# Performance work log

Hardware: AMD Instinct MI355X
Metric: run time of the kernel (lower is better)

## Reference

```python
import jax, jax.numpy as jnp
import numpy as np

B, S, D, N, NC = 2, 1024, 1024, 8192, 8


def _srw_chunked(x, h, emb_norm, tau_offset, w_read, w_write, n_chunks):
    Bd, Sd, Dd = x.shape
    Nd = emb_norm.shape[0]
    cs = Nd // n_chunks
    h_bf = h.astype(jnp.bfloat16)
    x_bf = x.astype(jnp.bfloat16)
    emb_bf = emb_norm.astype(jnp.bfloat16)
    read_bf = w_read.astype(jnp.bfloat16)
    write_bf = w_write.astype(jnp.bfloat16)
    z1 = jnp.zeros((Bd, Sd, 1))

    @jax.checkpoint
    def estimate_stats(h, emb, nc_val):
        ec0 = jax.lax.dynamic_slice_in_dim(emb, 0, cs, axis=0)
        sc0 = h @ ec0.T
        s_sum = sc0.sum(axis=-1, keepdims=True).astype(jnp.float32) * nc_val
        sq_sum = (sc0 ** 2).sum(axis=-1, keepdims=True).astype(jnp.float32) * nc_val
        return (s_sum, sq_sum)

    s_sum, sq_sum = estimate_stats(h_bf, emb_bf, n_chunks)
    s_mean = s_sum / Nd
    s_std = jnp.sqrt(sq_sum / Nd - s_mean ** 2) + 1e-08
    tau = s_mean + tau_offset * s_std
    tau_bf = tau.astype(jnp.bfloat16)

    @jax.checkpoint
    def gsrw_step(carry, i):
        out, es, em, ac, lbs, lbq = carry
        s = i * cs
        ec = jax.lax.dynamic_slice_in_dim(emb_bf, s, cs, axis=0)
        rc = jax.lax.dynamic_slice_in_dim(read_bf, s, cs, axis=0)
        wc = jax.lax.dynamic_slice_in_dim(write_bf, s, cs, axis=0)
        sc = h_bf @ ec.T  # [B,S,cs]
        raw = sc - tau_bf
        gc = jnp.where(raw > 0, raw, (1e-06 * jnp.exp(jnp.clip(raw.astype(jnp.float32), -10.0, 0.0))).astype(jnp.bfloat16))
        gc = jnp.clip(gc, 0.0, 10.0)
        eg = (jnp.exp(gc.astype(jnp.float32)) - 1.0).astype(jnp.bfloat16)
        ef = eg.astype(jnp.float32)
        xr = x_bf @ rc.T  # [B,S,cs]
        co = ((eg * xr) @ wc).astype(jnp.float32)  # [B,S,D]
        gn = ef.mean(axis=(0, 1))
        lbs = lbs + gn.sum()
        lbq = lbq + (gn ** 2).sum()
        return ((out + co,
                 es + ef.sum(axis=-1, keepdims=True),
                 jnp.maximum(em, ef.max(axis=-1, keepdims=True)),
                 ac + (raw > 0).sum(axis=-1, keepdims=True).astype(jnp.float32),
                 lbs, lbq), None)

    z_scalar = jnp.float32(0.0)
    init = (jnp.zeros((Bd, Sd, Dd), dtype=jnp.float32), z1,
            jnp.full((Bd, Sd, 1), -1000000000.0), z1, z_scalar, z_scalar)
    (raw_out, tes, tem, tac, lb_sum, lb_sq), _ = jax.lax.scan(gsrw_step, init, jnp.arange(n_chunks))
    inv_es = (1.0 / (tes + 1e-08)).astype(jnp.bfloat16)
    gs = jnp.tanh(tem).astype(jnp.bfloat16)
    out = raw_out * inv_es * gs
    exp_sum_scalar = tes.mean() + 1e-08
    norm_lb_sum = lb_sum / exp_sum_scalar
    norm_lb_sq = lb_sq / exp_sum_scalar ** 2
    lb_loss = norm_lb_sq * Nd - 2.0 * norm_lb_sum + 1.0
    gs_mean = jnp.tanh(tem).mean()
    es_mean = tes.mean()
    return (out.astype(jnp.float32), tac / Nd, tem, lb_loss, gs_mean, es_mean)


def setup_inputs() -> dict:
    key = jax.random.key(0)
    k = jax.random.split(key, 6)
    x = jax.random.normal(k[0], (B, S, D), jnp.float32)
    h = jax.random.normal(k[1], (B, S, D), jnp.float32)
    emb = jax.random.normal(k[2], (N, D), jnp.float32) * 0.02
    w_read = jax.random.normal(k[3], (N, D), jnp.float32) * 0.02
    w_write = jax.random.normal(k[4], (N, D), jnp.float32) * 0.02
    tau_offset = jax.random.normal(k[5], (B, S, 1), jnp.float32) * 0.1
    return {"x": x, "h": h, "emb": emb, "tau_offset": tau_offset,
            "w_read": w_read, "w_write": w_write, "n_chunks": NC}


def reference(x, h, emb, tau_offset, w_read, w_write, n_chunks):
    # caller (_know_forward) unit-normalizes the embedding pool first
    emb_norm = emb / (jnp.linalg.norm(emb, axis=-1, keepdims=True) + 1e-08)
    out, active_frac, gate_max, lb_loss, gs_mean, es_mean = _srw_chunked(
        x, h, emb_norm, tau_offset, w_read, w_write, n_chunks)
    return out
```

## Files before the change

kernel.cpp:

```cpp
#include <hip/hip_runtime.h>


#define MDIM 2048
#define DDIM 1024
#define NDIM 8192

typedef __attribute__((ext_vector_type(8))) __bf16 bf16x8;
typedef __attribute__((ext_vector_type(4))) float f32x4;

static __device__ __forceinline__ unsigned short f2b(float f) {
  unsigned u = __float_as_uint(f);
  u = (u + 0x7FFFu + ((u >> 16) & 1u)) >> 16;
  return (unsigned short)u;
}
static __device__ __forceinline__ float b2f(unsigned short s) {
  return __uint_as_float(((unsigned)s) << 16);
}


static __device__ __forceinline__ void stage_half(const unsigned short* __restrict__ src,
                                                  int ld, int row0, int k0,
                                                  char* lds, int lds_off, int w, int l) {
  const int rsub = l >> 3;
  const int col = k0 + 8 * ((l & 7) ^ rsub);
#pragma unroll
  for (int j = 0; j < 2; ++j) {
    const unsigned short* g =
        src + (size_t)(row0 + w * 8 + j * 64 + rsub) * (size_t)ld + col;
    __builtin_amdgcn_global_load_lds(
        (const __attribute__((address_space(1))) unsigned int*)(const void*)g,
        (__attribute__((address_space(3))) unsigned int*)(void*)(lds + lds_off + j * 8192 + w * 1024),
        16, 0, 0);
  }
}

#define LDSF(off) (*(const bf16x8*)(lds + (off)))
#define MFMA_BF16 __builtin_amdgcn_mfma_f32_16x16x32_bf16

static __device__ __forceinline__ void gemm256(const unsigned short* __restrict__ asrc,
                                               const unsigned short* __restrict__ bsrc,
                                               int ld, int m0, int n0, int kbase,
                                               char* lds, f32x4 (&acc)[8][4],
                                               int w, int l, int wr, int wc) {
  const int lrow = l & 15, lk = l >> 4;
  const int axor = (l & 7) << 4;
  const int kx0 = (lk << 4) ^ axor;
  const int kx1 = (64 | (lk << 4)) ^ axor;
  const int arow_off = lrow * 128;
  const int brow_off = ((wc & 1) * 64 + lrow) * 128;

  stage_half(asrc, ld, m0,       kbase,      lds, 0,             w, l);
  stage_half(asrc, ld, m0 + 128, kbase,      lds, 16384,         w, l);
  stage_half(bsrc, ld, n0,       kbase,      lds, 32768,         w, l);
  stage_half(bsrc, ld, n0 + 128, kbase,      lds, 49152,         w, l);
  stage_half(bsrc, ld, n0,       kbase + 64, lds, 65536 + 32768, w, l);
  stage_half(bsrc, ld, n0 + 128, kbase + 64, lds, 65536 + 49152, w, l);
  asm volatile("s_waitcnt vmcnt(4)" ::: "memory");
  __builtin_amdgcn_s_barrier();

  bf16x8 a[4][2], blo[2][2], bhi[2][2];
#pragma unroll 2
  for (int s = 0; s < 16; ++s) {
    const int ab = (s & 1) * 65536 + wr * 16384;
    const int bb = (s & 1) * 65536 + 32768 + (wc >> 1) * 16384;
#pragma unroll
    for (int m = 0; m < 4; ++m) {
      a[m][0] = LDSF(ab + arow_off + m * 2048 + kx0);
      a[m][1] = LDSF(ab + arow_off + m * 2048 + kx1);
    }
#pragma unroll
    for (int n = 0; n < 2; ++n) {
      blo[n][0] = LDSF(bb + brow_off + n * 2048 + kx0);
      blo[n][1] = LDSF(bb + brow_off + n * 2048 + kx1);
    }
    if (s + 1 < 16)
      stage_half(asrc, ld, m0, kbase + (s + 1) * 64, lds, ((s + 1) & 1) * 65536, w, l);
    asm volatile("s_waitcnt lgkmcnt(8)" ::: "memory");
    __builtin_amdgcn_s_barrier();
    asm volatile("s_waitcnt lgkmcnt(0)" ::: "memory");
    __builtin_amdgcn_s_setprio(1);
#pragma unroll
    for (int ks = 0; ks < 2; ++ks)
#pragma unroll
      for (int n = 0; n < 2; ++n)
#pragma unroll
        for (int m = 0; m < 4; ++m)
          acc[m][n] = MFMA_BF16(a[m][ks], blo[n][ks], acc[m][n], 0, 0, 0);
    __builtin_amdgcn_s_setprio(0);
    __builtin_amdgcn_s_barrier();
#pragma unroll
    for (int n = 0; n < 2; ++n) {
      bhi[n][0] = LDSF(bb + brow_off + (n + 2) * 2048 + kx0);
      bhi[n][1] = LDSF(bb + brow_off + (n + 2) * 2048 + kx1);
    }
    if (s + 1 < 16)
      stage_half(asrc, ld, m0 + 128, kbase + (s + 1) * 64, lds,
                 ((s + 1) & 1) * 65536 + 16384, w, l);
    __builtin_amdgcn_s_barrier();
    asm volatile("s_waitcnt lgkmcnt(0)" ::: "memory");
    __builtin_amdgcn_s_setprio(1);
#pragma unroll
    for (int ks = 0; ks < 2; ++ks)
#pragma unroll
      for (int n = 0; n < 2; ++n)
#pragma unroll
        for (int m = 0; m < 4; ++m)
          acc[m][n + 2] = MFMA_BF16(a[m][ks], bhi[n][ks], acc[m][n + 2], 0, 0, 0);
    __builtin_amdgcn_s_setprio(0);
    __builtin_amdgcn_s_barrier();
#pragma unroll
    for (int m = 0; m < 4; ++m) {
      a[m][0] = LDSF(ab + arow_off + (m + 4) * 2048 + kx0);
      a[m][1] = LDSF(ab + arow_off + (m + 4) * 2048 + kx1);
    }
    if (s + 2 < 16)
      stage_half(bsrc, ld, n0, kbase + (s + 2) * 64, lds, (s & 1) * 65536 + 32768, w, l);
    __builtin_amdgcn_s_barrier();
    asm volatile("s_waitcnt lgkmcnt(0)" ::: "memory");
    __builtin_amdgcn_s_setprio(1);
#pragma unroll
    for (int ks = 0; ks < 2; ++ks)
#pragma unroll
      for (int n = 0; n < 2; ++n)
#pragma unroll
        for (int m = 0; m < 4; ++m)
          acc[m + 4][n + 2] = MFMA_BF16(a[m][ks], bhi[n][ks], acc[m + 4][n + 2], 0, 0, 0);
    __builtin_amdgcn_s_setprio(0);
    __builtin_amdgcn_s_barrier();
    if (s + 2 < 16)
      stage_half(bsrc, ld, n0 + 128, kbase + (s + 2) * 64, lds, (s & 1) * 65536 + 49152, w, l);
    __builtin_amdgcn_s_barrier();
    asm volatile("s_waitcnt lgkmcnt(0)" ::: "memory");
    __builtin_amdgcn_s_setprio(1);
#pragma unroll
    for (int ks = 0; ks < 2; ++ks)
#pragma unroll
      for (int n = 0; n < 2; ++n)
#pragma unroll
        for (int m = 0; m < 4; ++m)
          acc[m + 4][n] = MFMA_BF16(a[m][ks], blo[n][ks], acc[m + 4][n], 0, 0, 0);
    __builtin_amdgcn_s_setprio(0);
    if (s <= 13) {
      asm volatile("s_waitcnt vmcnt(4)" ::: "memory");
    } else if (s == 14) {
      asm volatile("s_waitcnt vmcnt(0)" ::: "memory");
    }
    __builtin_amdgcn_s_barrier();
  }
}


__global__ __launch_bounds__(256) void k_norm(const float* __restrict__ emb,
                                              unsigned short* __restrict__ eb) {
  const int n = blockIdx.x, t = threadIdx.x;
  const float4 v = ((const float4*)(emb + (size_t)n * 1024))[t];
  float ss = v.x * v.x + v.y * v.y + v.z * v.z + v.w * v.w;
#pragma unroll
  for (int off = 1; off < 64; off <<= 1) ss += __shfl_xor(ss, off, 64);
  __shared__ float wsum[4];
  if ((t & 63) == 0) wsum[t >> 6] = ss;
  __syncthreads();
  const float tot = wsum[0] + wsum[1] + wsum[2] + wsum[3];
  const float denom = sqrtf(tot) + 1e-8f;
  ushort4 o;
  o.x = f2b(v.x / denom);
  o.y = f2b(v.y / denom);
  o.z = f2b(v.z / denom);
  o.w = f2b(v.w / denom);
  ((ushort4*)(eb + (size_t)n * 1024))[t] = o;
}

__global__ __launch_bounds__(256) void k_cast(const float* __restrict__ in,
                                              unsigned short* __restrict__ out, int n4) {
  const int i = blockIdx.x * 256 + threadIdx.x;
  if (i >= n4) return;
  const float4 v = ((const float4*)in)[i];
  ushort4 o;
  o.x = f2b(v.x);
  o.y = f2b(v.y);
  o.z = f2b(v.z);
  o.w = f2b(v.w);
  ((ushort4*)out)[i] = o;
}

__global__ __launch_bounds__(256) void k_twt(const float* __restrict__ w,
                                             unsigned short* __restrict__ wbT) {
  __shared__ float tsm[64][65];
  const int nb = blockIdx.x, db = blockIdx.y, t = threadIdx.x;
  const int r = t >> 2, c4 = (t & 3) * 16;
#pragma unroll
  for (int j = 0; j < 4; ++j) {
    const float4 v = *(const float4*)&w[(size_t)(nb * 64 + r) * 1024 + db * 64 + c4 + 4 * j];
    tsm[r][c4 + 4 * j + 0] = v.x;
    tsm[r][c4 + 4 * j + 1] = v.y;
    tsm[r][c4 + 4 * j + 2] = v.z;
    tsm[r][c4 + 4 * j + 3] = v.w;
  }
  __syncthreads();
  const int dr = t >> 2, nc0 = (t & 3) * 16;
  unsigned pk[8];
#pragma unroll
  for (int j = 0; j < 8; ++j) {
    const unsigned lo = f2b(tsm[nc0 + 2 * j][dr]);
    const unsigned hi = f2b(tsm[nc0 + 2 * j + 1][dr]);
    pk[j] = lo | (hi << 16);
  }
  uint4* dst = (uint4*)(wbT + (size_t)(db * 64 + dr) * 8192 + nb * 64 + nc0);
  uint4 w0, w1;
  w0.x = pk[0]; w0.y = pk[1]; w0.z = pk[2]; w0.w = pk[3];
  w1.x = pk[4]; w1.y = pk[5]; w1.z = pk[6]; w1.w = pk[7];
  dst[0] = w0;
  dst[1] = w1;
}


template <int TROWS>
static __device__ __forceinline__ void stage_tile(const unsigned short* __restrict__ src,
                                                  int row0, int k0, int ld,
                                                  unsigned short* lds, int wave, int lane) {
  const int rsub = lane >> 3;
  const int csub = (lane & 7) << 3;
#pragma unroll
  for (int q = 0; q < TROWS / 32; ++q) {
    const int p = q * 4 + wave;
    const unsigned short* g =
        src + (size_t)(row0 + p * 8 + rsub) * (size_t)ld + (size_t)(k0 + csub);
    __builtin_amdgcn_global_load_lds(
        (const __attribute__((address_space(1))) unsigned int*)(const void*)g,
        (__attribute__((address_space(3))) unsigned int*)(void*)(lds + p * 512),
        16, 0, 0);
  }
}

static __device__ __forceinline__ void gemm_128_128(const unsigned short* __restrict__ asrc,
                                                    const unsigned short* __restrict__ bsrc,
                                                    int m0, int n0, int K, int lda, int ldb,
                                                    unsigned short* a_sm, unsigned short* b_sm,
                                                    f32x4 (&acc)[4][4], int wave, int lane,
                                                    int wr, int wc) {
  const int arow = lane & 15;
  const int kcol = (lane >> 4) << 3;
  for (int k0 = 0; k0 < K; k0 += 64) {
    stage_tile<128>(asrc, m0, k0, lda, a_sm, wave, lane);
    stage_tile<128>(bsrc, n0, k0, ldb, b_sm, wave, lane);
    asm volatile("s_waitcnt vmcnt(0)" ::: "memory");
    __syncthreads();
#pragma unroll
    for (int ks = 0; ks < 2; ++ks) {
      bf16x8 af[4], bfr[4];
#pragma unroll
      for (int m = 0; m < 4; ++m)
        af[m] = *(const bf16x8*)&a_sm[(wr * 64 + m * 16 + arow) * 64 + ks * 32 + kcol];
#pragma unroll
      for (int n = 0; n < 4; ++n)
        bfr[n] = *(const bf16x8*)&b_sm[(wc * 64 + n * 16 + arow) * 64 + ks * 32 + kcol];
#pragma unroll
      for (int m = 0; m < 4; ++m)
#pragma unroll
        for (int n = 0; n < 4; ++n)
          acc[m][n] = MFMA_BF16(af[m], bfr[n], acc[m][n], 0, 0, 0);
    }
    __syncthreads();
  }
}

__global__ __launch_bounds__(256, 2) void k_stats(const unsigned short* __restrict__ hb,
                                                  const unsigned short* __restrict__ eb,
                                                  float* __restrict__ stat_s,
                                                  float* __restrict__ stat_q) {
  __shared__ unsigned short a_sm[128 * 64];
  __shared__ unsigned short b_sm[128 * 64];
  __shared__ float red_s[2][128];
  __shared__ float red_q[2][128];
  const int t = threadIdx.x;
  const int wave = t >> 6, lane = t & 63;
  const int wr = wave >> 1, wc = wave & 1;
  const int m0 = blockIdx.x * 128, n0 = blockIdx.y * 128;
  f32x4 acc[4][4];
#pragma unroll
  for (int m = 0; m < 4; ++m)
#pragma unroll
    for (int n = 0; n < 4; ++n) acc[m][n] = (f32x4)0.0f;
  gemm_128_128(hb, eb, m0, n0, 1024, 1024, 1024, a_sm, b_sm, acc, wave, lane, wr, wc);

  float s_r[4][4], q_r[4][4];
#pragma unroll
  for (int m = 0; m < 4; ++m)
#pragma unroll
    for (int i = 0; i < 4; ++i) { s_r[m][i] = 0.f; q_r[m][i] = 0.f; }
#pragma unroll
  for (int m = 0; m < 4; ++m)
#pragma unroll
    for (int n = 0; n < 4; ++n)
#pragma unroll
      for (int i = 0; i < 4; ++i) {
        const float scf = b2f(f2b(acc[m][n][i]));
        s_r[m][i] += scf;
        q_r[m][i] += b2f(f2b(scf * scf));
      }
#pragma unroll
  for (int m = 0; m < 4; ++m)
#pragma unroll
    for (int i = 0; i < 4; ++i) {
      float s = s_r[m][i], q = q_r[m][i];
      for (int off = 1; off < 16; off <<= 1) {
        s += __shfl_xor(s, off, 64);
        q += __shfl_xor(q, off, 64);
      }
      if ((lane & 15) == 0) {
        const int rloc = wr * 64 + m * 16 + (lane >> 4) * 4 + i;
        red_s[wc][rloc] = s;
        red_q[wc][rloc] = q;
      }
    }
  __syncthreads();
  if (t < 128) {
    stat_s[(size_t)(m0 + t) * 8 + blockIdx.y] = red_s[0][t] + red_s[1][t];
    stat_q[(size_t)(m0 + t) * 8 + blockIdx.y] = red_q[0][t] + red_q[1][t];
  }
}

__global__ void k_tau(const float* __restrict__ stat_s, const float* __restrict__ stat_q,
                      const float* __restrict__ tau_off, float* __restrict__ tau) {
  const int r = blockIdx.x * 256 + threadIdx.x;
  if (r >= MDIM) return;
  float S = 0.f, Q = 0.f;
#pragma unroll
  for (int j = 0; j < 8; ++j) {
    S += stat_s[(size_t)r * 8 + j];
    Q += stat_q[(size_t)r * 8 + j];
  }
  const float s_sum = S * 8.0f;
  const float sq_sum = Q * 8.0f;
  const float mean = s_sum * (1.0f / 8192.0f);
  const float var = __fsub_rn(sq_sum * (1.0f / 8192.0f), __fmul_rn(mean, mean));
  const float sd = __fadd_rn(__fsqrt_rn(var), 1e-8f);
  const float tv = __fadd_rn(mean, __fmul_rn(tau_off[r], sd));
  tau[r] = b2f(f2b(tv));
}


__global__ __launch_bounds__(512, 2) void k_sc(const unsigned short* __restrict__ hb,
                                               const unsigned short* __restrict__ eb,
                                               const float* __restrict__ tau,
                                               unsigned short* __restrict__ Aeg,
                                               float* __restrict__ es_part,
                                               float* __restrict__ em_part) {
  __shared__ __align__(16) char lds[131072];
  const int t = threadIdx.x, w = t >> 6, l = t & 63;
  const int wr = w >> 2, wc = w & 3;
  const int bid = blockIdx.x;
  const int swz = (bid & 7) * 32 + (bid >> 3);
  const int m0 = (swz >> 5) * 256, n0 = (swz & 31) * 256;
  f32x4 acc[8][4];
#pragma unroll
  for (int m = 0; m < 8; ++m)
#pragma unroll
    for (int n = 0; n < 4; ++n) acc[m][n] = (f32x4)0.0f;
  gemm256(hb, eb, 1024, m0, n0, 0, lds, acc, w, l, wr, wc);

  __syncthreads();
  float* tau_sm = (float*)lds;
  float* red_es = (float*)(lds + 1024);
  float* red_em = (float*)(lds + 1024 + 4096);
  if (t < 256) tau_sm[t] = tau[m0 + t];
  __syncthreads();
  const int lrow = l & 15, lk = l >> 4;
#pragma unroll
  for (int m = 0; m < 8; ++m) {
#pragma unroll
    for (int i = 0; i < 4; ++i) {
      const int rl = wr * 128 + m * 16 + lk * 4 + i;
      const float taub = tau_sm[rl];
      float es_v = 0.f, em_v = 0.f;
#pragma unroll
      for (int n = 0; n < 4; ++n) {
        const float scf = b2f(f2b(acc[m][n][i]));
        const float rawf = b2f(f2b(scf - taub));
        float gcf;
        if (rawf > 0.f) gcf = fminf(rawf, 10.0f);
        else gcf = b2f(f2b(1e-6f * expf(fmaxf(rawf, -10.0f))));
        const unsigned short egu = f2b(expf(gcf) - 1.0f);
        const float ef = b2f(egu);
        es_v += ef;
        em_v = fmaxf(em_v, ef);
        Aeg[(size_t)(m0 + rl) * NDIM + (size_t)(n0 + wc * 64 + n * 16 + lrow)] = egu;
      }
      for (int off = 1; off < 16; off <<= 1) {
        es_v += __shfl_xor(es_v, off, 64);
        em_v = fmaxf(em_v, __shfl_xor(em_v, off, 64));
      }
      if (lrow == 0) {
        red_es[wc * 256 + rl] = es_v;
        red_em[wc * 256 + rl] = em_v;
      }
    }
  }
  __syncthreads();
  if (t < 256) {
    const float s = red_es[t] + red_es[256 + t] + red_es[512 + t] + red_es[768 + t];
    const float e = fmaxf(fmaxf(red_em[t], red_em[256 + t]),
                          fmaxf(red_em[512 + t], red_em[768 + t]));
    es_part[(size_t)(m0 + t) * 32 + (n0 >> 8)] = s;
    em_part[(size_t)(m0 + t) * 32 + (n0 >> 8)] = e;
  }
}


__global__ __launch_bounds__(512, 2) void k_xr(const unsigned short* __restrict__ xb,
                                               const unsigned short* __restrict__ rb,
                                               unsigned short* __restrict__ Aeg) {
  __shared__ __align__(16) char lds[131072];
  const int t = threadIdx.x, w = t >> 6, l = t & 63;
  const int wr = w >> 2, wc = w & 3;
  const int bid = blockIdx.x;
  const int swz = (bid & 7) * 32 + (bid >> 3);
  const int m0 = (swz >> 5) * 256, n0 = (swz & 31) * 256;
  f32x4 acc[8][4];
#pragma unroll
  for (int m = 0; m < 8; ++m)
#pragma unroll
    for (int n = 0; n < 4; ++n) acc[m][n] = (f32x4)0.0f;
  gemm256(xb, rb, 1024, m0, n0, 0, lds, acc, w, l, wr, wc);

  const int lrow = l & 15, lk = l >> 4;
#pragma unroll
  for (int m = 0; m < 8; ++m)
#pragma unroll
    for (int n = 0; n < 4; ++n)
#pragma unroll
      for (int i = 0; i < 4; ++i) {
        const int rl = wr * 128 + m * 16 + lk * 4 + i;
        const size_t idx =
            (size_t)(m0 + rl) * NDIM + (size_t)(n0 + wc * 64 + n * 16 + lrow);
        const unsigned short egu = Aeg[idx];
        const float xrf = b2f(f2b(acc[m][n][i]));
        Aeg[idx] = f2b(b2f(egu) * xrf);
      }
}


__global__ __launch_bounds__(512, 2) void k_out(const unsigned short* __restrict__ A,
                                                const unsigned short* __restrict__ wbT,
                                                unsigned short* __restrict__ pacc) {
  __shared__ __align__(16) char lds[131072];
  const int t = threadIdx.x, w = t >> 6, l = t & 63;
  const int wr = w >> 2, wc = w & 3;
  const int bid = blockIdx.x;
  const int swz = (bid & 7) * 32 + (bid >> 3);
  const int bm = swz >> 5, chunk = (swz >> 2) & 7, bd = swz & 3;
  const int m0 = bm * 256, d0 = bd * 256;
  f32x4 acc[8][4];
#pragma unroll
  for (int m = 0; m < 8; ++m)
#pragma unroll
    for (int n = 0; n < 4; ++n) acc[m][n] = (f32x4)0.0f;
  gemm256(A, wbT, 8192, m0, d0, chunk * 1024, lds, acc, w, l, wr, wc);

  const int lrow = l & 15, lk = l >> 4;
#pragma unroll
  for (int m = 0; m < 8; ++m)
#pragma unroll
    for (int n = 0; n < 4; ++n)
#pragma unroll
      for (int i = 0; i < 4; ++i) {
        const int rl = wr * 128 + m * 16 + lk * 4 + i;
        pacc[((size_t)chunk * MDIM + (m0 + rl)) * DDIM +
             (size_t)(d0 + wc * 64 + n * 16 + lrow)] = f2b(acc[m][n][i]);
      }
}


__global__ void k_scale(const float* __restrict__ es_part, const float* __restrict__ em_part,
                        float* __restrict__ scale2) {
  const int r = blockIdx.x * 256 + threadIdx.x;
  if (r >= MDIM) return;
  float s = 0.f, m = 0.f;
#pragma unroll
  for (int j = 0; j < 32; ++j) {
    s += es_part[(size_t)r * 32 + j];
    m = fmaxf(m, em_part[(size_t)r * 32 + j]);
  }
  scale2[2 * r] = b2f(f2b(1.0f / (s + 1e-8f)));
  scale2[2 * r + 1] = b2f(f2b(tanhf(m)));
}

__global__ __launch_bounds__(256) void k_finish(const unsigned short* __restrict__ pacc,
                                                const float* __restrict__ scale2,
                                                float* __restrict__ outp) {
  const int t = blockIdx.x * 256 + threadIdx.x;
  const int r = t >> 8;
  const int d4 = (t & 255) * 4;
  float sx = 0.f, sy = 0.f, sz = 0.f, sw = 0.f;
#pragma unroll
  for (int c = 0; c < 8; ++c) {
    const ushort4 v = *(const ushort4*)(pacc + ((size_t)c * MDIM + r) * DDIM + d4);
    sx += b2f(v.x);
    sy += b2f(v.y);
    sz += b2f(v.z);
    sw += b2f(v.w);
  }
  const float inv = scale2[2 * r];
  const float gsv = scale2[2 * r + 1];
  float4 o;
  o.x = (sx * inv) * gsv;
  o.y = (sy * inv) * gsv;
  o.z = (sz * inv) * gsv;
  o.w = (sw * inv) * gsv;
  *(float4*)(outp + (size_t)r * DDIM + d4) = o;
}


extern "C" void kernel_launch(void* const* d_in, const int* in_sizes, int n_in,
                              void* d_out, int out_size, void* d_ws, size_t ws_size,
                              hipStream_t stream) {
  const float* x = (const float*)d_in[0];
  const float* h = (const float*)d_in[1];
  const float* emb = (const float*)d_in[2];
  const float* tau_off = (const float*)d_in[3];
  const float* w_read = (const float*)d_in[4];
  const float* w_write = (const float*)d_in[5];

  char* ws = (char*)d_ws;
  const size_t MB = 1024 * 1024;
  unsigned short* rb = (unsigned short*)(ws);
  unsigned short* eb = (unsigned short*)(ws + 16 * MB);
  unsigned short* wbT = (unsigned short*)(ws + 32 * MB);
  unsigned short* hb = (unsigned short*)(ws + 48 * MB);
  unsigned short* xb = (unsigned short*)(ws + 52 * MB);
  unsigned short* Aeg = (unsigned short*)(ws + 56 * MB);
  unsigned short* pacc = (unsigned short*)(ws);
  float* tau = (float*)(ws + 88 * MB);
  float* stat_s = (float*)(ws + 88 * MB + 1 * 65536);
  float* stat_q = (float*)(ws + 88 * MB + 2 * 65536);
  float* es_part = (float*)(ws + 88 * MB + 3 * 65536);
  float* em_part = (float*)(ws + 88 * MB + 7 * 65536);
  float* scale2 = (float*)(ws + 88 * MB + 11 * 65536);
  if (ws_size < 88 * MB + 12 * 65536) return;
  float* outp = (float*)d_out;

  k_norm<<<NDIM, 256, 0, stream>>>(emb, eb);
  k_cast<<<(NDIM * DDIM / 4) / 256, 256, 0, stream>>>(w_read, rb, NDIM * DDIM / 4);
  k_cast<<<(MDIM * DDIM / 4) / 256, 256, 0, stream>>>(h, hb, MDIM * DDIM / 4);
  k_cast<<<(MDIM * DDIM / 4) / 256, 256, 0, stream>>>(x, xb, MDIM * DDIM / 4);
  k_twt<<<dim3(NDIM / 64, DDIM / 64), 256, 0, stream>>>(w_write, wbT);
  k_stats<<<dim3(MDIM / 128, 8), 256, 0, stream>>>(hb, eb, stat_s, stat_q);
  k_tau<<<MDIM / 256, 256, 0, stream>>>(stat_s, stat_q, tau_off, tau);
  k_sc<<<256, 512, 0, stream>>>(hb, eb, tau, Aeg, es_part, em_part);
  k_scale<<<MDIM / 256, 256, 0, stream>>>(es_part, em_part, scale2);
  k_xr<<<256, 512, 0, stream>>>(xb, rb, Aeg);
  k_out<<<256, 512, 0, stream>>>(Aeg, wbT, pacc);
  k_finish<<<(MDIM * DDIM / 4) / 256, 256, 0, stream>>>(pacc, scale2, outp);
}
```

Before: 212.0 us.

## Fuse prep kernels, merge score and read GEMMs, restructure GEMM main loop

```diff
diff --git a/kernel.cpp b/kernel.cpp
--- a/kernel.cpp
+++ b/kernel.cpp
@@ -17,6 +17,8 @@
   return __uint_as_float(((unsigned)s) << 16);
 }
 
+#define LDSF(off) (*(const bf16x8*)(lds + (off)))
+#define MFMA_BF16 __builtin_amdgcn_mfma_f32_16x16x32_bf16
 
 static __device__ __forceinline__ void stage_half(const unsigned short* __restrict__ src,
                                                   int ld, int row0, int k0,
@@ -34,8 +36,91 @@
   }
 }
 
-#define LDSF(off) (*(const bf16x8*)(lds + (off)))
-#define MFMA_BF16 __builtin_amdgcn_mfma_f32_16x16x32_bf16
+template <int PAR, bool SA, bool SB, int VMC>
+static __device__ __forceinline__ void ktile(const unsigned short* __restrict__ asrc,
+                                             const unsigned short* __restrict__ bsrc,
+                                             int ld, int m0, int n0, int kA, int kB,
+                                             char* lds, f32x4 (&acc)[8][4],
+                                             int w, int l, int wr, int wc,
+                                             int arow_off, int brow_off, int kx0, int kx1) {
+  const int ab = PAR * 65536 + wr * 16384;
+  const int bb = PAR * 65536 + 32768 + (wc >> 1) * 16384;
+  const int nxt = (1 - PAR) * 65536;
+  bf16x8 a[4][2], blo[2][2], bhi[2][2];
+  if (SA) stage_half(asrc, ld, m0, kA, lds, nxt, w, l);
+#pragma unroll
+  for (int m = 0; m < 4; ++m) {
+    a[m][0] = LDSF(ab + arow_off + m * 2048 + kx0);
+    a[m][1] = LDSF(ab + arow_off + m * 2048 + kx1);
+  }
+#pragma unroll
+  for (int n = 0; n < 2; ++n) {
+    blo[n][0] = LDSF(bb + brow_off + n * 2048 + kx0);
+    blo[n][1] = LDSF(bb + brow_off + n * 2048 + kx1);
+  }
+  asm volatile("s_waitcnt lgkmcnt(8)" ::: "memory");
+  __builtin_amdgcn_s_barrier();
+  asm volatile("s_waitcnt lgkmcnt(0)" ::: "memory");
+  __builtin_amdgcn_s_setprio(1);
+#pragma unroll
+  for (int ks = 0; ks < 2; ++ks)
+#pragma unroll
+    for (int n = 0; n < 2; ++n)
+#pragma unroll
+      for (int m = 0; m < 4; ++m)
+        acc[m][n] = MFMA_BF16(a[m][ks], blo[n][ks], acc[m][n], 0, 0, 0);
+  __builtin_amdgcn_s_setprio(0);
+  __builtin_amdgcn_s_barrier();
+  if (SA) stage_half(asrc, ld, m0 + 128, kA, lds, nxt + 16384, w, l);
+#pragma unroll
+  for (int n = 0; n < 2; ++n) {
+    bhi[n][0] = LDSF(bb + brow_off + (n + 2) * 2048 + kx0);
+    bhi[n][1] = LDSF(bb + brow_off + (n + 2) * 2048 + kx1);
+  }
+  __builtin_amdgcn_s_barrier();
+  asm volatile("s_waitcnt lgkmcnt(0)" ::: "memory");
+  __builtin_amdgcn_s_setprio(1);
+#pragma unroll
+  for (int ks = 0; ks < 2; ++ks)
+#pragma unroll
+    for (int n = 0; n < 2; ++n)
+#pragma unroll
+      for (int m = 0; m < 4; ++m)
+        acc[m][n + 2] = MFMA_BF16(a[m][ks], bhi[n][ks], acc[m][n + 2], 0, 0, 0);
+  __builtin_amdgcn_s_setprio(0);
+  __builtin_amdgcn_s_barrier();
+  if (SB) stage_half(bsrc, ld, n0, kB, lds, PAR * 65536 + 32768, w, l);
+#pragma unroll
+  for (int m = 0; m < 4; ++m) {
+    a[m][0] = LDSF(ab + arow_off + (m + 4) * 2048 + kx0);
+    a[m][1] = LDSF(ab + arow_off + (m + 4) * 2048 + kx1);
+  }
+  __builtin_amdgcn_s_barrier();
+  asm volatile("s_waitcnt lgkmcnt(0)" ::: "memory");
+  __builtin_amdgcn_s_setprio(1);
+#pragma unroll
+  for (int ks = 0; ks < 2; ++ks)
+#pragma unroll
+    for (int n = 0; n < 2; ++n)
+#pragma unroll
+      for (int m = 0; m < 4; ++m)
+        acc[m + 4][n + 2] = MFMA_BF16(a[m][ks], bhi[n][ks], acc[m + 4][n + 2], 0, 0, 0);
+  __builtin_amdgcn_s_setprio(0);
+  __builtin_amdgcn_s_barrier();
+  if (SB) stage_half(bsrc, ld, n0 + 128, kB, lds, PAR * 65536 + 49152, w, l);
+  __builtin_amdgcn_s_setprio(1);
+#pragma unroll
+  for (int ks = 0; ks < 2; ++ks)
+#pragma unroll
+    for (int n = 0; n < 2; ++n)
+#pragma unroll
+      for (int m = 0; m < 4; ++m)
+        acc[m + 4][n] = MFMA_BF16(a[m][ks], blo[n][ks], acc[m + 4][n], 0, 0, 0);
+  __builtin_amdgcn_s_setprio(0);
+  if (VMC == 4) asm volatile("s_waitcnt vmcnt(4)" ::: "memory");
+  if (VMC == 0) asm volatile("s_waitcnt vmcnt(0)" ::: "memory");
+  __builtin_amdgcn_s_barrier();
+}
 
 static __device__ __forceinline__ void gemm256(const unsigned short* __restrict__ asrc,
                                                const unsigned short* __restrict__ bsrc,
@@ -58,159 +143,91 @@
   asm volatile("s_waitcnt vmcnt(4)" ::: "memory");
   __builtin_amdgcn_s_barrier();
 
-  bf16x8 a[4][2], blo[2][2], bhi[2][2];
-#pragma unroll 2
-  for (int s = 0; s < 16; ++s) {
-    const int ab = (s & 1) * 65536 + wr * 16384;
-    const int bb = (s & 1) * 65536 + 32768 + (wc >> 1) * 16384;
-#pragma unroll
-    for (int m = 0; m < 4; ++m) {
-      a[m][0] = LDSF(ab + arow_off + m * 2048 + kx0);
-      a[m][1] = LDSF(ab + arow_off + m * 2048 + kx1);
+#pragma unroll 1
+  for (int s = 0; s < 14; s += 2) {
+    ktile<0, true, true, 4>(asrc, bsrc, ld, m0, n0, kbase + (s + 1) * 64,
+                            kbase + (s + 2) * 64, lds, acc, w, l, wr, wc,
+                            arow_off, brow_off, kx0, kx1);
+    ktile<1, true, true, 4>(asrc, bsrc, ld, m0, n0, kbase + (s + 2) * 64,
+                            kbase + (s + 3) * 64, lds, acc, w, l, wr, wc,
+                            arow_off, brow_off, kx0, kx1);
+  }
+  ktile<0, true, false, 0>(asrc, bsrc, ld, m0, n0, kbase + 15 * 64, 0, lds, acc,
+                           w, l, wr, wc, arow_off, brow_off, kx0, kx1);
+  ktile<1, false, false, -1>(asrc, bsrc, ld, m0, n0, 0, 0, lds, acc,
+                             w, l, wr, wc, arow_off, brow_off, kx0, kx1);
+}
+
+
+__global__ __launch_bounds__(256) void k_prep(const float* __restrict__ emb,
+                                              const float* __restrict__ w_read,
+                                              const float* __restrict__ h,
+                                              const float* __restrict__ x,
+                                              const float* __restrict__ w_write,
+                                              unsigned short* __restrict__ eb,
+                                              unsigned short* __restrict__ rb,
+                                              unsigned short* __restrict__ hb,
+                                              unsigned short* __restrict__ xb,
+                                              unsigned short* __restrict__ wbT) {
+  const int b = blockIdx.x, t = threadIdx.x;
+  if (b < 8192) {
+    const float4 v = ((const float4*)(emb + (size_t)b * 1024))[t];
+    float ss = v.x * v.x + v.y * v.y + v.z * v.z + v.w * v.w;
+#pragma unroll
+    for (int off = 1; off < 64; off <<= 1) ss += __shfl_xor(ss, off, 64);
+    __shared__ float wsum[4];
+    if ((t & 63) == 0) wsum[t >> 6] = ss;
+    __syncthreads();
+    const float denom = sqrtf(wsum[0] + wsum[1] + wsum[2] + wsum[3]) + 1e-8f;
+    ushort4 o;
+    o.x = f2b(v.x / denom);
+    o.y = f2b(v.y / denom);
+    o.z = f2b(v.z / denom);
+    o.w = f2b(v.w / denom);
+    ((ushort4*)(eb + (size_t)b * 1024))[t] = o;
+  } else if (b < 20480) {
+    const float* src;
+    unsigned short* dst;
+    int i;
+    if (b < 16384) { src = w_read; dst = rb; i = (b - 8192) * 256 + t; }
+    else if (b < 18432) { src = h; dst = hb; i = (b - 16384) * 256 + t; }
+    else { src = x; dst = xb; i = (b - 18432) * 256 + t; }
+    const float4 v = ((const float4*)src)[i];
+    ushort4 o;
+    o.x = f2b(v.x);
+    o.y = f2b(v.y);
+    o.z = f2b(v.z);
+    o.w = f2b(v.w);
+    ((ushort4*)dst)[i] = o;
+  } else {
+    __shared__ float tsm[64][65];
+    const int b2 = b - 20480;
+    const int nb = b2 & 127, db = b2 >> 7;
+    const int r = t >> 2, c4 = (t & 3) * 16;
+#pragma unroll
+    for (int j = 0; j < 4; ++j) {
+      const float4 v = *(const float4*)&w_write[(size_t)(nb * 64 + r) * 1024 + db * 64 + c4 + 4 * j];
+      tsm[r][c4 + 4 * j + 0] = v.x;
+      tsm[r][c4 + 4 * j + 1] = v.y;
+      tsm[r][c4 + 4 * j + 2] = v.z;
+      tsm[r][c4 + 4 * j + 3] = v.w;
     }
-#pragma unroll
-    for (int n = 0; n < 2; ++n) {
-      blo[n][0] = LDSF(bb + brow_off + n * 2048 + kx0);
-      blo[n][1] = LDSF(bb + brow_off + n * 2048 + kx1);
+    __syncthreads();
+    const int dr = t >> 2, nc0 = (t & 3) * 16;
+    unsigned pk[8];
+#pragma unroll
+    for (int j = 0; j < 8; ++j) {
+      const unsigned lo = f2b(tsm[nc0 + 2 * j][dr]);
+      const unsigned hi = f2b(tsm[nc0 + 2 * j + 1][dr]);
+      pk[j] = lo | (hi << 16);
     }
-    if (s + 1 < 16)
-      stage_half(asrc, ld, m0, kbase + (s + 1) * 64, lds, ((s + 1) & 1) * 65536, w, l);
-    asm volatile("s_waitcnt lgkmcnt(8)" ::: "memory");
-    __builtin_amdgcn_s_barrier();
-    asm volatile("s_waitcnt lgkmcnt(0)" ::: "memory");
-    __builtin_amdgcn_s_setprio(1);
-#pragma unroll
-    for (int ks = 0; ks < 2; ++ks)
-#pragma unroll
-      for (int n = 0; n < 2; ++n)
-#pragma unroll
-        for (int m = 0; m < 4; ++m)
-          acc[m][n] = MFMA_BF16(a[m][ks], blo[n][ks], acc[m][n], 0, 0, 0);
-    __builtin_amdgcn_s_setprio(0);
-    __builtin_amdgcn_s_barrier();
-#pragma unroll
-    for (int n = 0; n < 2; ++n) {
-      bhi[n][0] = LDSF(bb + brow_off + (n + 2) * 2048 + kx0);
-      bhi[n][1] = LDSF(bb + brow_off + (n + 2) * 2048 + kx1);
-    }
-    if (s + 1 < 16)
-      stage_half(asrc, ld, m0 + 128, kbase + (s + 1) * 64, lds,
-                 ((s + 1) & 1) * 65536 + 16384, w, l);
-    __builtin_amdgcn_s_barrier();
-    asm volatile("s_waitcnt lgkmcnt(0)" ::: "memory");
-    __builtin_amdgcn_s_setprio(1);
-#pragma unroll
-    for (int ks = 0; ks < 2; ++ks)
-#pragma unroll
-      for (int n = 0; n < 2; ++n)
-#pragma unroll
-        for (int m = 0; m < 4; ++m)
-          acc[m][n + 2] = MFMA_BF16(a[m][ks], bhi[n][ks], acc[m][n + 2], 0, 0, 0);
-    __builtin_amdgcn_s_setprio(0);
-    __builtin_amdgcn_s_barrier();
-#pragma unroll
-    for (int m = 0; m < 4; ++m) {
-      a[m][0] = LDSF(ab + arow_off + (m + 4) * 2048 + kx0);
-      a[m][1] = LDSF(ab + arow_off + (m + 4) * 2048 + kx1);
-    }
-    if (s + 2 < 16)
-      stage_half(bsrc, ld, n0, kbase + (s + 2) * 64, lds, (s & 1) * 65536 + 32768, w, l);
-    __builtin_amdgcn_s_barrier();
-    asm volatile("s_waitcnt lgkmcnt(0)" ::: "memory");
-    __builtin_amdgcn_s_setprio(1);
-#pragma unroll
-    for (int ks = 0; ks < 2; ++ks)
-#pragma unroll
-      for (int n = 0; n < 2; ++n)
-#pragma unroll
-        for (int m = 0; m < 4; ++m)
-          acc[m + 4][n + 2] = MFMA_BF16(a[m][ks], bhi[n][ks], acc[m + 4][n + 2], 0, 0, 0);
-    __builtin_amdgcn_s_setprio(0);
-    __builtin_amdgcn_s_barrier();
-    if (s + 2 < 16)
-      stage_half(bsrc, ld, n0 + 128, kbase + (s + 2) * 64, lds, (s & 1) * 65536 + 49152, w, l);
-    __builtin_amdgcn_s_barrier();
-    asm volatile("s_waitcnt lgkmcnt(0)" ::: "memory");
-    __builtin_amdgcn_s_setprio(1);
-#pragma unroll
-    for (int ks = 0; ks < 2; ++ks)
-#pragma unroll
-      for (int n = 0; n < 2; ++n)
-#pragma unroll
-        for (int m = 0; m < 4; ++m)
-          acc[m + 4][n] = MFMA_BF16(a[m][ks], blo[n][ks], acc[m + 4][n], 0, 0, 0);
-    __builtin_amdgcn_s_setprio(0);
-    if (s <= 13) {
-      asm volatile("s_waitcnt vmcnt(4)" ::: "memory");
-    } else if (s == 14) {
-      asm volatile("s_waitcnt vmcnt(0)" ::: "memory");
-    }
-    __builtin_amdgcn_s_barrier();
-  }
-}
-
-
-__global__ __launch_bounds__(256) void k_norm(const float* __restrict__ emb,
-                                              unsigned short* __restrict__ eb) {
-  const int n = blockIdx.x, t = threadIdx.x;
-  const float4 v = ((const float4*)(emb + (size_t)n * 1024))[t];
-  float ss = v.x * v.x + v.y * v.y + v.z * v.z + v.w * v.w;
-#pragma unroll
-  for (int off = 1; off < 64; off <<= 1) ss += __shfl_xor(ss, off, 64);
-  __shared__ float wsum[4];
-  if ((t & 63) == 0) wsum[t >> 6] = ss;
-  __syncthreads();
-  const float tot = wsum[0] + wsum[1] + wsum[2] + wsum[3];
-  const float denom = sqrtf(tot) + 1e-8f;
-  ushort4 o;
-  o.x = f2b(v.x / denom);
-  o.y = f2b(v.y / denom);
-  o.z = f2b(v.z / denom);
-  o.w = f2b(v.w / denom);
-  ((ushort4*)(eb + (size_t)n * 1024))[t] = o;
-}
-
-__global__ __launch_bounds__(256) void k_cast(const float* __restrict__ in,
-                                              unsigned short* __restrict__ out, int n4) {
-  const int i = blockIdx.x * 256 + threadIdx.x;
-  if (i >= n4) return;
-  const float4 v = ((const float4*)in)[i];
-  ushort4 o;
-  o.x = f2b(v.x);
-  o.y = f2b(v.y);
-  o.z = f2b(v.z);
-  o.w = f2b(v.w);
-  ((ushort4*)out)[i] = o;
-}
-
-__global__ __launch_bounds__(256) void k_twt(const float* __restrict__ w,
-                                             unsigned short* __restrict__ wbT) {
-  __shared__ float tsm[64][65];
-  const int nb = blockIdx.x, db = blockIdx.y, t = threadIdx.x;
-  const int r = t >> 2, c4 = (t & 3) * 16;
-#pragma unroll
-  for (int j = 0; j < 4; ++j) {
-    const float4 v = *(const float4*)&w[(size_t)(nb * 64 + r) * 1024 + db * 64 + c4 + 4 * j];
-    tsm[r][c4 + 4 * j + 0] = v.x;
-    tsm[r][c4 + 4 * j + 1] = v.y;
-    tsm[r][c4 + 4 * j + 2] = v.z;
-    tsm[r][c4 + 4 * j + 3] = v.w;
-  }
-  __syncthreads();
-  const int dr = t >> 2, nc0 = (t & 3) * 16;
-  unsigned pk[8];
-#pragma unroll
-  for (int j = 0; j < 8; ++j) {
-    const unsigned lo = f2b(tsm[nc0 + 2 * j][dr]);
-    const unsigned hi = f2b(tsm[nc0 + 2 * j + 1][dr]);
-    pk[j] = lo | (hi << 16);
-  }
-  uint4* dst = (uint4*)(wbT + (size_t)(db * 64 + dr) * 8192 + nb * 64 + nc0);
-  uint4 w0, w1;
-  w0.x = pk[0]; w0.y = pk[1]; w0.z = pk[2]; w0.w = pk[3];
-  w1.x = pk[4]; w1.y = pk[5]; w1.z = pk[6]; w1.w = pk[7];
-  dst[0] = w0;
-  dst[1] = w1;
+    uint4* dst = (uint4*)(wbT + (size_t)(db * 64 + dr) * 8192 + nb * 64 + nc0);
+    uint4 w0, w1;
+    w0.x = pk[0]; w0.y = pk[1]; w0.z = pk[2]; w0.w = pk[3];
+    w1.x = pk[4]; w1.y = pk[5]; w1.z = pk[6]; w1.w = pk[7];
+    dst[0] = w0;
+    dst[1] = w1;
+  }
 }
 
 
@@ -229,38 +246,6 @@
         (const __attribute__((address_space(1))) unsigned int*)(const void*)g,
         (__attribute__((address_space(3))) unsigned int*)(void*)(lds + p * 512),
         16, 0, 0);
-  }
-}
-
-static __device__ __forceinline__ void gemm_128_128(const unsigned short* __restrict__ asrc,
-                                                    const unsigned short* __restrict__ bsrc,
-                                                    int m0, int n0, int K, int lda, int ldb,
-                                                    unsigned short* a_sm, unsigned short* b_sm,
-                                                    f32x4 (&acc)[4][4], int wave, int lane,
-                                                    int wr, int wc) {
-  const int arow = lane & 15;
-  const int kcol = (lane >> 4) << 3;
-  for (int k0 = 0; k0 < K; k0 += 64) {
-    stage_tile<128>(asrc, m0, k0, lda, a_sm, wave, lane);
-    stage_tile<128>(bsrc, n0, k0, ldb, b_sm, wave, lane);
-    asm volatile("s_waitcnt vmcnt(0)" ::: "memory");
-    __syncthreads();
-#pragma unroll
-    for (int ks = 0; ks < 2; ++ks) {
-      bf16x8 af[4], bfr[4];
-#pragma unroll
-      for (int m = 0; m < 4; ++m)
-        af[m] = *(const bf16x8*)&a_sm[(wr * 64 + m * 16 + arow) * 64 + ks * 32 + kcol];
-#pragma unroll
-      for (int n = 0; n < 4; ++n)
-        bfr[n] = *(const bf16x8*)&b_sm[(wc * 64 + n * 16 + arow) * 64 + ks * 32 + kcol];
-#pragma unroll
-      for (int m = 0; m < 4; ++m)
-#pragma unroll
-        for (int n = 0; n < 4; ++n)
-          acc[m][n] = MFMA_BF16(af[m], bfr[n], acc[m][n], 0, 0, 0);
-    }
-    __syncthreads();
   }
 }
 
@@ -276,12 +261,35 @@
   const int wave = t >> 6, lane = t & 63;
   const int wr = wave >> 1, wc = wave & 1;
   const int m0 = blockIdx.x * 128, n0 = blockIdx.y * 128;
+  const int arow = lane & 15;
+  const int kcol = (lane >> 4) << 3;
   f32x4 acc[4][4];
 #pragma unroll
   for (int m = 0; m < 4; ++m)
 #pragma unroll
     for (int n = 0; n < 4; ++n) acc[m][n] = (f32x4)0.0f;
-  gemm_128_128(hb, eb, m0, n0, 1024, 1024, 1024, a_sm, b_sm, acc, wave, lane, wr, wc);
+  for (int k0 = 0; k0 < 1024; k0 += 64) {
+    stage_tile<128>(hb, m0, k0, 1024, a_sm, wave, lane);
+    stage_tile<128>(eb, n0, k0, 1024, b_sm, wave, lane);
+    asm volatile("s_waitcnt vmcnt(0)" ::: "memory");
+    __syncthreads();
+#pragma unroll
+    for (int ks = 0; ks < 2; ++ks) {
+      bf16x8 af[4], bfr[4];
+#pragma unroll
+      for (int m = 0; m < 4; ++m)
+        af[m] = *(const bf16x8*)&a_sm[(wr * 64 + m * 16 + arow) * 64 + ks * 32 + kcol];
+#pragma unroll
+      for (int n = 0; n < 4; ++n)
+        bfr[n] = *(const bf16x8*)&b_sm[(wc * 64 + n * 16 + arow) * 64 + ks * 32 + kcol];
+#pragma unroll
+      for (int m = 0; m < 4; ++m)
+#pragma unroll
+        for (int n = 0; n < 4; ++n)
+          acc[m][n] = MFMA_BF16(af[m], bfr[n], acc[m][n], 0, 0, 0);
+    }
+    __syncthreads();
+  }
 
   float s_r[4][4], q_r[4][4];
 #pragma unroll
@@ -340,18 +348,22 @@
 }
 
 
-__global__ __launch_bounds__(512, 2) void k_sc(const unsigned short* __restrict__ hb,
-                                               const unsigned short* __restrict__ eb,
-                                               const float* __restrict__ tau,
-                                               unsigned short* __restrict__ Aeg,
-                                               float* __restrict__ es_part,
-                                               float* __restrict__ em_part) {
+__global__ __launch_bounds__(512, 2) void k_gate(const unsigned short* __restrict__ hb,
+                                                 const unsigned short* __restrict__ eb,
+                                                 const unsigned short* __restrict__ xb,
+                                                 const unsigned short* __restrict__ rb,
+                                                 const float* __restrict__ tau,
+                                                 unsigned short* __restrict__ Aeg,
+                                                 float* __restrict__ es_part,
+                                                 float* __restrict__ em_part) {
   __shared__ __align__(16) char lds[131072];
   const int t = threadIdx.x, w = t >> 6, l = t & 63;
   const int wr = w >> 2, wc = w & 3;
   const int bid = blockIdx.x;
   const int swz = (bid & 7) * 32 + (bid >> 3);
   const int m0 = (swz >> 5) * 256, n0 = (swz & 31) * 256;
+  const int lrow = l & 15, lk = l >> 4;
+
   f32x4 acc[8][4];
 #pragma unroll
   for (int m = 0; m < 8; ++m)
@@ -365,7 +377,6 @@
   float* red_em = (float*)(lds + 1024 + 4096);
   if (t < 256) tau_sm[t] = tau[m0 + t];
   __syncthreads();
-  const int lrow = l & 15, lk = l >> 4;
 #pragma unroll
   for (int m = 0; m < 8; ++m) {
 #pragma unroll
@@ -404,26 +415,14 @@
     es_part[(size_t)(m0 + t) * 32 + (n0 >> 8)] = s;
     em_part[(size_t)(m0 + t) * 32 + (n0 >> 8)] = e;
   }
-}
-
-
-__global__ __launch_bounds__(512, 2) void k_xr(const unsigned short* __restrict__ xb,
-                                               const unsigned short* __restrict__ rb,
-                                               unsigned short* __restrict__ Aeg) {
-  __shared__ __align__(16) char lds[131072];
-  const int t = threadIdx.x, w = t >> 6, l = t & 63;
-  const int wr = w >> 2, wc = w & 3;
-  const int bid = blockIdx.x;
-  const int swz = (bid & 7) * 32 + (bid >> 3);
-  const int m0 = (swz >> 5) * 256, n0 = (swz & 31) * 256;
-  f32x4 acc[8][4];
+  __syncthreads();
+
 #pragma unroll
   for (int m = 0; m < 8; ++m)
 #pragma unroll
     for (int n = 0; n < 4; ++n) acc[m][n] = (f32x4)0.0f;
   gemm256(xb, rb, 1024, m0, n0, 0, lds, acc, w, l, wr, wc);
 
-  const int lrow = l & 15, lk = l >> 4;
 #pragma unroll
   for (int m = 0; m < 8; ++m)
 #pragma unroll
@@ -539,16 +538,11 @@
   if (ws_size < 88 * MB + 12 * 65536) return;
   float* outp = (float*)d_out;
 
-  k_norm<<<NDIM, 256, 0, stream>>>(emb, eb);
-  k_cast<<<(NDIM * DDIM / 4) / 256, 256, 0, stream>>>(w_read, rb, NDIM * DDIM / 4);
-  k_cast<<<(MDIM * DDIM / 4) / 256, 256, 0, stream>>>(h, hb, MDIM * DDIM / 4);
-  k_cast<<<(MDIM * DDIM / 4) / 256, 256, 0, stream>>>(x, xb, MDIM * DDIM / 4);
-  k_twt<<<dim3(NDIM / 64, DDIM / 64), 256, 0, stream>>>(w_write, wbT);
+  k_prep<<<22528, 256, 0, stream>>>(emb, w_read, h, x, w_write, eb, rb, hb, xb, wbT);
   k_stats<<<dim3(MDIM / 128, 8), 256, 0, stream>>>(hb, eb, stat_s, stat_q);
   k_tau<<<MDIM / 256, 256, 0, stream>>>(stat_s, stat_q, tau_off, tau);
-  k_sc<<<256, 512, 0, stream>>>(hb, eb, tau, Aeg, es_part, em_part);
+  k_gate<<<256, 512, 0, stream>>>(hb, eb, xb, rb, tau, Aeg, es_part, em_part);
   k_scale<<<MDIM / 256, 256, 0, stream>>>(es_part, em_part, scale2);
-  k_xr<<<256, 512, 0, stream>>>(xb, rb, Aeg);
   k_out<<<256, 512, 0, stream>>>(Aeg, wbT, pacc);
   k_finish<<<(MDIM * DDIM / 4) / 256, 256, 0, stream>>>(pacc, scale2, outp);
 }
```

Measured after the change: 224.9 us. 6.1% more time.
